# Optimization experiments

Measured on AMD Instinct MI355X. Metric: run time of the kernel, lower is better.

## Reference

```python
import jax, jax.numpy as jnp
import numpy as np

DT = 0.001  # integration time step (forward arg dt in the original module)


def force_fn(x):
    # Harmonic well stand-in for the user-supplied force function.
    return -x


def _nh_step(x, v, alpha, kT, mass, Q):
    """One Nose-Hoover step, exactly mirroring the recompute block in backward()."""
    ndof = x.shape[-1]
    v2 = (v * v).sum(-1)
    alpha = alpha + (DT / 4) * (v2 - ndof * kT) / Q
    v = v * jnp.exp(-alpha[..., None] * (DT / 2))
    v2 = (v * v).sum(-1)
    alpha = alpha + (DT / 4) * (v2 - ndof * kT) / Q
    v = v + (DT / 2) * force_fn(x) / mass
    x = x + DT * v
    v = v + (DT / 2) * force_fn(x) / mass
    v2 = (v * v).sum(-1)
    alpha = alpha + (DT / 4) * (v2 - ndof * kT) / Q
    v = v * jnp.exp(-alpha[..., None] * (DT / 2))
    v2 = (v * v).sum(-1)
    alpha = alpha + (DT / 4) * (v2 - ndof * kT) / Q
    return x, v, alpha


def setup_inputs() -> dict:
    key = jax.random.key(0)
    k1, k2 = jax.random.split(key)
    B, D = 4096, 64  # batch of systems, degrees of freedom per system
    return {
        "x0": jax.random.normal(k1, (B, D), jnp.float32),
        "v0": jax.random.normal(k2, (B, D), jnp.float32),
        "alpha0": jnp.zeros((B,), jnp.float32),
        "kT": jnp.ones((), jnp.float32),
        "mass": jnp.ones((), jnp.float32),
        "Q": jnp.ones((), jnp.float32),
        "n_steps": 1000,
        "store_every": 10,
    }


def reference(x0, v0, alpha0, kT, mass, Q, n_steps, store_every):
    n_chunks = n_steps // store_every  # assume divisibility (1000 / 10)

    def inner(c, _):
        x, v, a = c
        return _nh_step(x, v, a, kT, mass, Q), None

    def chunk(c, _):
        c, _ = jax.lax.scan(inner, c, None, length=store_every)
        return c, (c[0], c[1])  # snapshot (x, v) every store_every steps

    _, (xs, vs) = jax.lax.scan(chunk, (x0, v0, alpha0), None, length=n_chunks)
    traj_x = jnp.concatenate([x0[None], xs], axis=0)  # [n_steps//store_every + 1, B, D]
    traj_v = jnp.concatenate([v0[None], vs], axis=0)
    return traj_x, traj_v
```

## Files before the change

kernel.cpp:

```cpp
#include <hip/hip_runtime.h>

#define DT 0.001f

typedef float f4 __attribute__((ext_vector_type(4)));

__device__ __forceinline__ float sumsq(const f4 a) {
    return (a.x * a.x + a.y * a.y) + (a.z * a.z + a.w * a.w);
}
__device__ __forceinline__ float dot4(const f4 a, const f4 b) {
    return (a.x * b.x + a.y * b.y) + (a.z * b.z + a.w * b.w);
}

template<int SE>
__global__ __launch_bounds__(64) void nh_scalar(
    const float* __restrict__ x0, const float* __restrict__ v0,
    const float* __restrict__ alpha0,
    const float* __restrict__ kT_p, const float* __restrict__ mass_p,
    const float* __restrict__ Q_p,
    const int* __restrict__ n_steps_p, const int* __restrict__ store_every_p,
    float* __restrict__ out, int B)
{
    const int sys = blockIdx.x * 64 + threadIdx.x;
    if (sys >= B) return;

    const int n_steps = *n_steps_p;
    const int se_rt   = *store_every_p;
    const int se      = (SE > 0) ? SE : se_rt;
    const int n_chunks = n_steps / se_rt;

    const int D = 64;
    const float kt = *kT_p, m = *mass_p, q = *Q_p;
    const float c   = 0.25f * DT / q;
    const float E   = (float)D * kt;
    const float cE  = c * E;
    const float c2  = 2.0f * c;
    const float c2E = 2.0f * cE;
    const float M2C2E = -2.0f * c2E;
    const float hd  = 0.5f * DT / m;
    const float hdt = 0.5f * DT;

    const float A11 = 1.0f - hd * DT;
    const float A21 = -hd * (2.0f - hd * DT);
    const float Ph1 = -hdt, Ph2 = 0.5f * hdt * hdt;
    const float Pf1 = -DT,  Pf2 = 0.5f * DT * DT;
    const float kc1 = -c2 * DT;
    const float kc2 = 0.5f * c2 * DT * DT;
    const float G00 = 1.0f - Ph1 * c2E;
    const float G01 = Ph1 * c2;
    const float G10 = 2.0f * Ph1;
    const float G11 = Ph1 * kc1;
    const float G2P = 4.0f * Ph2;

    const f4* xr = (const f4*)x0 + (size_t)sys * 16;
    const f4* vr = (const f4*)v0 + (size_t)sys * 16;
    float Sxx = 0.f, Sxv = 0.f, Svv = 0.f;
    #pragma unroll
    for (int j = 0; j < 16; ++j) {
        const f4 a = xr[j], bv = vr[j];
        Sxx += sumsq(a);
        Svv += sumsq(bv);
        Sxv += dot4(a, bv);
    }
    float tSxv = 2.0f * Sxv;

    const float al0 = alpha0[sys];
    const float a1  = __builtin_fmaf(c, Svv, al0 - cE);
    float sv  = __builtin_fmaf(a1, __builtin_fmaf(a1, Ph2, Ph1), 1.0f);
    const float s1q = __builtin_fmaf(a1, __builtin_fmaf(a1, Pf2, Pf1), 1.0f);
    const float r1 = Svv * s1q;
    float alm = __builtin_fmaf(c, r1, a1 - c2E);

    float pc00 = 1.f, pc01 = 0.f, pc10 = 0.f, pc11 = 1.f;

    f4* outx = (f4*)out;
    const int snap4 = B * 16;

    for (int ck = 1; ck <= n_chunks; ++ck) {
        float m00 = 1.f, m01 = 0.f, m10 = 0.f, m11 = 1.f;
        float q0 = A11, q1 = 0.f, p0 = A21, p1 = 0.f;
        #pragma unroll
        for (int i = 0; i < se - 1; ++i) {
            const float b = sv * DT;
            const float d = sv * A11;
            const float n00 = __builtin_fmaf(b, m10, q0);
            const float n01 = __builtin_fmaf(b, m11, q1);
            const float n10 = __builtin_fmaf(d, m10, p0);
            const float n11 = __builtin_fmaf(d, m11, p1);
            const float u1 = __builtin_fmaf(tSxv, n11, Sxx * n10);
            const float r  = __builtin_fmaf(Svv, n11 * n11, n10 * u1);
            const float a3 = __builtin_fmaf(c, r, alm);
            const float g0 = __builtin_fmaf(G01, r, G00);
            const float g1 = __builtin_fmaf(G11, r, G10);
            const float svn = __builtin_fmaf(a3, __builtin_fmaf(a3, G2P, g1), g0);
            const float k0m = __builtin_fmaf(c2, r, M2C2E);
            const float k1  = __builtin_fmaf(kc1, r, 1.0f);
            const float k2  = kc2 * r;
            const float a4m = __builtin_fmaf(a3, __builtin_fmaf(a3, k2, k1), k0m);
            alm = __builtin_fmaf(c * r, svn * svn, a4m);
            m00 = n00; m01 = n01; m10 = n10; m11 = n11;
            q0 = A11 * n00; q1 = A11 * n01;
            p0 = A21 * n00; p1 = A21 * n01;
            sv = svn;
        }
        const float b = sv * DT;
        const float d = sv * A11;
        const float n00 = __builtin_fmaf(b, m10, q0);
        const float n01 = __builtin_fmaf(b, m11, q1);
        const float n10 = __builtin_fmaf(d, m10, p0);
        const float n11 = __builtin_fmaf(d, m11, p1);
        const float u1 = __builtin_fmaf(tSxv, n11, Sxx * n10);
        const float r  = __builtin_fmaf(Svv, n11 * n11, n10 * u1);
        const float a3 = __builtin_fmaf(c, r, alm);
        const float s2  = __builtin_fmaf(a3, __builtin_fmaf(a3, Ph2, Ph1), 1.0f);
        const float s2q = __builtin_fmaf(a3, __builtin_fmaf(a3, Pf2, Pf1), 1.0f);
        const float w2 = s2 * n10;
        const float w3 = s2 * n11;
        const float t00 = __builtin_fmaf(n00, pc00, n01 * pc10);
        const float t01 = __builtin_fmaf(n00, pc01, n01 * pc11);
        const float t10 = __builtin_fmaf(w2,  pc00, w3  * pc10);
        const float t11 = __builtin_fmaf(w2,  pc01, w3  * pc11);
        pc00 = t00; pc01 = t01; pc10 = t10; pc11 = t11;
        f4 P; P.x = pc00; P.y = pc01; P.z = pc10; P.w = pc11;
        outx[(size_t)ck * snap4 + (size_t)sys * 16] = P;
        const float SxxN = __builtin_fmaf(n00 * n00, Sxx,
                             __builtin_fmaf(n00 * n01, tSxv, n01 * n01 * Svv));
        const float SxvN = __builtin_fmaf(w2 * n00, Sxx,
                             __builtin_fmaf(0.5f * __builtin_fmaf(n00, w3, n01 * w2), tSxv,
                                            n01 * w3 * Svv));
        const float SvvN = r * s2q;
        const float aU4 = __builtin_fmaf(c, SvvN, a3 - cE);
        const float aU1 = __builtin_fmaf(c, SvvN, aU4 - cE);
        const float s1n  = __builtin_fmaf(aU1, __builtin_fmaf(aU1, Ph2, Ph1), 1.0f);
        const float s1qn = __builtin_fmaf(aU1, __builtin_fmaf(aU1, Pf2, Pf1), 1.0f);
        alm = __builtin_fmaf(c * SvvN, s1qn, aU1 - c2E);
        sv = s1n;
        Sxx = SxxN; tSxv = 2.0f * SxvN; Svv = SvvN;
    }
}

__global__ __launch_bounds__(256) void nh_apply(
    const float* __restrict__ x0, const float* __restrict__ v0,
    float* __restrict__ out, int B, int n_chunks)
{
    const int snap4 = B * 16;
    const int bpc = B >> 4;
    const int ck   = blockIdx.x / bpc;
    const int rem  = blockIdx.x - ck * bpc;
    const int fidx = rem * 256 + threadIdx.x;

    f4* outx = (f4*)out;
    f4* outv = outx + (size_t)(n_chunks + 1) * snap4;

    const f4 xv = ((const f4*)x0)[fidx];
    const f4 vv = ((const f4*)v0)[fidx];

    if (ck == 0) {
        __builtin_nontemporal_store(xv, &outx[fidx]);
        __builtin_nontemporal_store(vv, &outv[fidx]);
        return;
    }

    const int sys16 = fidx & ~15;
    const f4 P = outx[(size_t)ck * snap4 + sys16];
    const f4 xe = P.x * xv + P.y * vv;
    const f4 ve = P.z * xv + P.w * vv;
    __builtin_nontemporal_store(xe, &outx[(size_t)ck * snap4 + fidx]);
    __builtin_nontemporal_store(ve, &outv[(size_t)ck * snap4 + fidx]);
}

extern "C" void kernel_launch(void* const* d_in, const int* in_sizes, int n_in,
                              void* d_out, int out_size, void* d_ws, size_t ws_size,
                              hipStream_t stream) {
    const float* x0     = (const float*)d_in[0];
    const float* v0     = (const float*)d_in[1];
    const float* alpha0 = (const float*)d_in[2];
    const float* kT     = (const float*)d_in[3];
    const float* mass   = (const float*)d_in[4];
    const float* Q      = (const float*)d_in[5];
    const int* n_steps  = (const int*)d_in[6];
    const int* store_ev = (const int*)d_in[7];

    const int B = in_sizes[0] / 64;
    const int n_snap   = out_size / (B * 128);
    const int n_chunks = n_snap - 1;

    nh_scalar<10><<<(B + 63) / 64, 64, 0, stream>>>(
        x0, v0, alpha0, kT, mass, Q, n_steps, store_ev, (float*)d_out, B);

    const int bpc = B >> 4;
    nh_apply<<<n_snap * bpc, 256, 0, stream>>>(
        x0, v0, (float*)d_out, B, n_chunks);
}
```

Before: 319.1 us.

## Fuse scalar recurrence and snapshot apply into one kernel with 32 lanes per system

```diff
diff --git a/kernel.cpp b/kernel.cpp
--- a/kernel.cpp
+++ b/kernel.cpp
@@ -2,17 +2,19 @@
 
 #define DT 0.001f
 
-typedef float f4 __attribute__((ext_vector_type(4)));
+typedef float f2 __attribute__((ext_vector_type(2)));
 
-__device__ __forceinline__ float sumsq(const f4 a) {
-    return (a.x * a.x + a.y * a.y) + (a.z * a.z + a.w * a.w);
-}
-__device__ __forceinline__ float dot4(const f4 a, const f4 b) {
-    return (a.x * b.x + a.y * b.y) + (a.z * b.z + a.w * b.w);
+__device__ __forceinline__ float red32(float t) {
+    t += __shfl_xor(t, 1,  64);
+    t += __shfl_xor(t, 2,  64);
+    t += __shfl_xor(t, 4,  64);
+    t += __shfl_xor(t, 8,  64);
+    t += __shfl_xor(t, 16, 64);
+    return t;
 }
 
 template<int SE>
-__global__ __launch_bounds__(64) void nh_scalar(
+__global__ __launch_bounds__(256) void nh_fused(
     const float* __restrict__ x0, const float* __restrict__ v0,
     const float* __restrict__ alpha0,
     const float* __restrict__ kT_p, const float* __restrict__ mass_p,
@@ -20,7 +22,9 @@
     const int* __restrict__ n_steps_p, const int* __restrict__ store_every_p,
     float* __restrict__ out, int B)
 {
-    const int sys = blockIdx.x * 64 + threadIdx.x;
+    const int gid = blockIdx.x * 256 + threadIdx.x;
+    const int sys = gid >> 5;
+    const int g   = gid & 31;
     if (sys >= B) return;
 
     const int n_steps = *n_steps_p;
@@ -51,29 +55,31 @@
     const float G11 = Ph1 * kc1;
     const float G2P = 4.0f * Ph2;
 
-    const f4* xr = (const f4*)x0 + (size_t)sys * 16;
-    const f4* vr = (const f4*)v0 + (size_t)sys * 16;
-    float Sxx = 0.f, Sxv = 0.f, Svv = 0.f;
-    #pragma unroll
-    for (int j = 0; j < 16; ++j) {
-        const f4 a = xr[j], bv = vr[j];
-        Sxx += sumsq(a);
-        Svv += sumsq(bv);
-        Sxv += dot4(a, bv);
-    }
+    const int snapF2 = B * 32;
+    const int fidx   = sys * 32 + g;
+
+    const f2 xv = ((const f2*)x0)[fidx];
+    const f2 vv = ((const f2*)v0)[fidx];
+
+    f2* outx = (f2*)out;
+    f2* outv = outx + (size_t)(n_chunks + 1) * snapF2;
+
+    __builtin_nontemporal_store(xv, &outx[fidx]);
+    __builtin_nontemporal_store(vv, &outv[fidx]);
+
+    float Sxx = red32(xv.x * xv.x + xv.y * xv.y);
+    float Svv = red32(vv.x * vv.x + vv.y * vv.y);
+    float Sxv = red32(xv.x * vv.x + xv.y * vv.y);
     float tSxv = 2.0f * Sxv;
 
     const float al0 = alpha0[sys];
     const float a1  = __builtin_fmaf(c, Svv, al0 - cE);
     float sv  = __builtin_fmaf(a1, __builtin_fmaf(a1, Ph2, Ph1), 1.0f);
-    const float s1q = __builtin_fmaf(a1, __builtin_fmaf(a1, Pf2, Pf1), 1.0f);
-    const float r1 = Svv * s1q;
+    const float s1q0 = __builtin_fmaf(a1, __builtin_fmaf(a1, Pf2, Pf1), 1.0f);
+    const float r1 = Svv * s1q0;
     float alm = __builtin_fmaf(c, r1, a1 - c2E);
 
     float pc00 = 1.f, pc01 = 0.f, pc10 = 0.f, pc11 = 1.f;
-
-    f4* outx = (f4*)out;
-    const int snap4 = B * 16;
 
     for (int ck = 1; ck <= n_chunks; ++ck) {
         float m00 = 1.f, m01 = 0.f, m10 = 0.f, m11 = 1.f;
@@ -120,8 +126,10 @@
         const float t10 = __builtin_fmaf(w2,  pc00, w3  * pc10);
         const float t11 = __builtin_fmaf(w2,  pc01, w3  * pc11);
         pc00 = t00; pc01 = t01; pc10 = t10; pc11 = t11;
-        f4 P; P.x = pc00; P.y = pc01; P.z = pc10; P.w = pc11;
-        outx[(size_t)ck * snap4 + (size_t)sys * 16] = P;
+        const f2 xe = pc00 * xv + pc01 * vv;
+        const f2 ve = pc10 * xv + pc11 * vv;
+        __builtin_nontemporal_store(xe, &outx[(size_t)ck * snapF2 + fidx]);
+        __builtin_nontemporal_store(ve, &outv[(size_t)ck * snapF2 + fidx]);
         const float SxxN = __builtin_fmaf(n00 * n00, Sxx,
                              __builtin_fmaf(n00 * n01, tSxv, n01 * n01 * Svv));
         const float SxvN = __builtin_fmaf(w2 * n00, Sxx,
@@ -138,36 +146,6 @@
     }
 }
 
-__global__ __launch_bounds__(256) void nh_apply(
-    const float* __restrict__ x0, const float* __restrict__ v0,
-    float* __restrict__ out, int B, int n_chunks)
-{
-    const int snap4 = B * 16;
-    const int bpc = B >> 4;
-    const int ck   = blockIdx.x / bpc;
-    const int rem  = blockIdx.x - ck * bpc;
-    const int fidx = rem * 256 + threadIdx.x;
-
-    f4* outx = (f4*)out;
-    f4* outv = outx + (size_t)(n_chunks + 1) * snap4;
-
-    const f4 xv = ((const f4*)x0)[fidx];
-    const f4 vv = ((const f4*)v0)[fidx];
-
-    if (ck == 0) {
-        __builtin_nontemporal_store(xv, &outx[fidx]);
-        __builtin_nontemporal_store(vv, &outv[fidx]);
-        return;
-    }
-
-    const int sys16 = fidx & ~15;
-    const f4 P = outx[(size_t)ck * snap4 + sys16];
-    const f4 xe = P.x * xv + P.y * vv;
-    const f4 ve = P.z * xv + P.w * vv;
-    __builtin_nontemporal_store(xe, &outx[(size_t)ck * snap4 + fidx]);
-    __builtin_nontemporal_store(ve, &outv[(size_t)ck * snap4 + fidx]);
-}
-
 extern "C" void kernel_launch(void* const* d_in, const int* in_sizes, int n_in,
                               void* d_out, int out_size, void* d_ws, size_t ws_size,
                               hipStream_t stream) {
@@ -181,13 +159,10 @@
     const int* store_ev = (const int*)d_in[7];
 
     const int B = in_sizes[0] / 64;
-    const int n_snap   = out_size / (B * 128);
-    const int n_chunks = n_snap - 1;
+    const int threads = B * 32;
+    const int block = 256;
+    const int grid = (threads + block - 1) / block;
 
-    nh_scalar<10><<<(B + 63) / 64, 64, 0, stream>>>(
+    nh_fused<10><<<grid, block, 0, stream>>>(
         x0, v0, alpha0, kT, mass, Q, n_steps, store_ev, (float*)d_out, B);
-
-    const int bpc = B >> 4;
-    nh_apply<<<n_snap * bpc, 256, 0, stream>>>(
-        x0, v0, (float*)d_out, B, n_chunks);
 }
```

Result: faster. 288.3 us (-9.7%).
